# Optimization experiments

Hardware: AMD Instinct MI355X
Metric: run time of the kernel (lower is better)

Reference implementation:

```python
import jax, jax.numpy as jnp
import numpy as np


def setup_inputs() -> dict:
    key = jax.random.key(0)
    ks = jax.random.split(key, 12)
    B, N, Dv, E, H, V, T = 128, 196, 512, 512, 1024, 10000, 20
    s = 0.02  # small init scale for numerical stability
    f = lambda k, shp: (jax.random.normal(k, shp, jnp.float32) * s)
    return {
        "features": jax.random.normal(ks[0], (B, N, Dv), jnp.float32),
        "captions": jax.random.randint(ks[1], (B, T), 0, V),
        "W_init_h": f(ks[2], (H, Dv)),
        "W_init_c": f(ks[3], (H, Dv)),
        "W_attn_v": f(ks[4], (1, Dv)),
        "b_attn_v": jnp.zeros((1,), jnp.float32),
        "W_attn_h": f(ks[5], (1, H)),
        "b_attn_h": jnp.zeros((1,), jnp.float32),
        "embed_table": f(ks[6], (V, E)),
        "W_ih": f(ks[7], (4 * H, Dv + E)),
        "W_hh": f(ks[8], (4 * H, H)),
        "b_ih": jnp.zeros((4 * H,), jnp.float32),
        "b_hh": jnp.zeros((4 * H,), jnp.float32),
        "W_out": f(ks[9], (V, H)),
        "b_out": jnp.zeros((V,), jnp.float32),
    }


def reference(features, captions, W_init_h, W_init_c, W_attn_v, b_attn_v,
              W_attn_h, b_attn_h, embed_table, W_ih, W_hh, b_ih, b_hh,
              W_out, b_out):
    B, N, Dv = features.shape
    # _init_hidden: mean over vis_num of linear projections (division by vis_num)
    h0 = jnp.sum(jnp.einsum('bnd,hd->bnh', features, W_init_h), axis=1) / N
    c0 = jnp.sum(jnp.einsum('bnd,hd->bnh', features, W_init_c), axis=1) / N

    emb = embed_table[captions]                      # B,T,E
    emb_t_major = jnp.swapaxes(emb, 0, 1)            # T,B,E
    # visual attention logits are time-invariant; precompute once
    att_v = jnp.einsum('bnd,od->bno', features, W_attn_v) + b_attn_v  # B,N,1

    def step(carry, emb_t):
        h, c = carry
        # soft attention over vis_num locations
        att_h = (h @ W_attn_h.T + b_attn_h)[:, None, :]   # B,1,1
        alpha = jax.nn.softmax(att_v + att_h, axis=1)     # B,N,1
        ctx = jnp.sum(features * alpha, axis=1)           # B,Dv
        # single-step LSTM (PyTorch gate order: i, f, g, o)
        x = jnp.concatenate([ctx, emb_t], axis=-1)        # B,Dv+E
        gates = x @ W_ih.T + h @ W_hh.T + b_ih + b_hh     # B,4H
        i, fg, g, o = jnp.split(gates, 4, axis=-1)
        c_new = jax.nn.sigmoid(fg) * c + jax.nn.sigmoid(i) * jnp.tanh(g)
        h_new = jax.nn.sigmoid(o) * jnp.tanh(c_new)
        words = h_new @ W_out.T + b_out                   # B,V
        return (h_new, c_new), words

    _, word_space = jax.lax.scan(step, (h0, c0), emb_t_major)  # T,B,V
    # pack_padded_sequence with all-equal lengths flattens time-major -> (T*B, V)
    packed = word_space.reshape(-1, word_space.shape[-1])
    return jax.nn.log_softmax(packed, axis=1), jax.nn.softmax(packed, axis=1)
```

## Files before the change

### kernel.cpp

```cpp
#include <hip/hip_runtime.h>
#include <math.h>

#define B    128
#define NLOC 196
#define DV   512
#define EMB  512
#define HD   1024
#define VV   10000
#define TT   20
#define G4   4096
#define VPAD 10112
#define BH   (B*HD)

typedef short bf16x8 __attribute__((ext_vector_type(8)));
typedef float f32x4  __attribute__((ext_vector_type(4)));

__device__ __forceinline__ unsigned short f2bf(float x) {
    unsigned u = __builtin_bit_cast(unsigned, x);
    unsigned r = (u + 0x7fffu + ((u >> 16) & 1u)) >> 16;
    return (unsigned short)r;
}

__device__ __forceinline__ void gload_lds16(const void* g, void* lds) {
    __builtin_amdgcn_global_load_lds(
        (const __attribute__((address_space(1))) void*)g,
        (__attribute__((address_space(3))) void*)lds, 16, 0, 0);
}


__global__ void fmean_kernel(const float* __restrict__ feat, short* __restrict__ fmean_b) {
    int idx = blockIdx.x * blockDim.x + threadIdx.x;
    if (idx >= B * DV) return;
    int b = idx / DV, d = idx % DV;
    const float* p = feat + (size_t)b * NLOC * DV + d;
    float s = 0.f;
    for (int n = 0; n < NLOC; ++n) s += p[(size_t)n * DV];
    fmean_b[idx] = (short)f2bf(s * (1.0f / NLOC));
}

__global__ void attv_kernel(const float* __restrict__ feat, const float* __restrict__ wv,
                            const float* __restrict__ bv, float* __restrict__ attv) {
    int row  = blockIdx.x;
    int lane = threadIdx.x;
    const float* p = feat + (size_t)row * DV;
    float s = 0.f;
    for (int k = lane; k < DV; k += 64) s += p[k] * wv[k];
    for (int off = 32; off > 0; off >>= 1) s += __shfl_down(s, off);
    if (lane == 0) attv[row] = s + bv[0];
}

__global__ void alpha_kernel(const float* __restrict__ attv, float* __restrict__ alpha) {
    int b   = blockIdx.x;
    int tid = threadIdx.x;
    __shared__ float red[256];
    float v = (tid < NLOC) ? attv[b * NLOC + tid] : -1e30f;
    red[tid] = v; __syncthreads();
    for (int s = 128; s > 0; s >>= 1) { if (tid < s) red[tid] = fmaxf(red[tid], red[tid + s]); __syncthreads(); }
    float m = red[0]; __syncthreads();
    float e = (tid < NLOC) ? expf(v - m) : 0.f;
    red[tid] = e; __syncthreads();
    for (int s = 128; s > 0; s >>= 1) { if (tid < s) red[tid] += red[tid + s]; __syncthreads(); }
    float sum = red[0];
    if (tid < NLOC) alpha[b * NLOC + tid] = e / sum;
}

__global__ void ctx_kernel(const float* __restrict__ feat, const float* __restrict__ alpha,
                           short* __restrict__ ctx_b) {
    int idx = blockIdx.x * blockDim.x + threadIdx.x;
    if (idx >= B * DV) return;
    int b = idx / DV, d = idx % DV;
    const float* p = feat + (size_t)b * NLOC * DV + d;
    const float* a = alpha + b * NLOC;
    float s = 0.f;
    for (int n = 0; n < NLOC; ++n) s += a[n] * p[(size_t)n * DV];
    ctx_b[idx] = (short)f2bf(s);
}

__global__ void emb_gather_kernel(const int* __restrict__ captions, const float* __restrict__ table,
                                  short* __restrict__ emb_b) {
    size_t idx = (size_t)blockIdx.x * blockDim.x + threadIdx.x;
    if (idx >= (size_t)TT * B * EMB) return;
    int k = (int)(idx % EMB);
    int r = (int)(idx / EMB);
    int t = r / B, b = r % B;
    int cap = captions[b * TT + t];
    emb_b[idx] = (short)f2bf(table[(size_t)cap * EMB + k]);
}

__global__ void f2bf_pad_kernel(const float* __restrict__ in, short* __restrict__ out,
                                size_t n, size_t npad) {
    size_t i = (size_t)blockIdx.x * blockDim.x + threadIdx.x;
    if (i >= npad) return;
    out[i] = (i < n) ? (short)f2bf(in[i]) : (short)0;
}

__global__ void whh_perm_kernel(const float* __restrict__ in, short* __restrict__ out) {
    size_t idx = (size_t)blockIdx.x * blockDim.x + threadIdx.x;
    if (idx >= (size_t)G4 * HD) return;
    int k = (int)(idx & (HD - 1));
    int P = (int)(idx >> 10);
    int u = P >> 2, g = P & 3;
    out[idx] = (short)f2bf(in[(size_t)(g * HD + u) * HD + k]);
}

__global__ void hcvt_kernel(const float* __restrict__ h, short* __restrict__ h_bf) {
    int idx = blockIdx.x * blockDim.x + threadIdx.x;
    if (idx >= B * HD) return;
    h_bf[idx] = (short)f2bf(h[idx]);
}

template<int BN, int WR, int WC>
__global__ __launch_bounds__(256)
void gemm_bf16(const short* __restrict__ A, const short* __restrict__ Bw,
               float* __restrict__ C,
               const float* __restrict__ bias0, const float* __restrict__ bias1,
               int M, int N, int K, int lda, int ldb, int ldc) {
    constexpr int BM = 128;
    constexpr int BK = 32;
    constexpr int WM = BM / WR;
    constexpr int WN = BN / WC;
    constexpr int FM = WM / 16;
    constexpr int FN = WN / 16;
    __shared__ __align__(16) short As[BM * BK];
    __shared__ __align__(16) short Bs[BN * BK];
    const int tid  = threadIdx.x;
    const int wave = tid >> 6, lane = tid & 63;
    const int wr = wave / WC, wc = wave % WC;
    const int m0 = blockIdx.y * BM, n0 = blockIdx.x * BN;
    const int laneoff = lane * 16;

    f32x4 acc[FM][FN] = {};

    for (int k0 = 0; k0 < K; k0 += BK) {
        #pragma unroll
        for (int r = 0; r < 2; ++r) {
            int o   = r * 4096 + wave * 1024 + laneoff;
            int row = o >> 6;
            int col = (o & 63) >> 1;
            gload_lds16(A + (size_t)(m0 + row) * lda + k0 + col,
                        (char*)As + r * 4096 + wave * 1024);
        }
        constexpr int BBYTES = BN * BK * 2;
        if constexpr (BBYTES >= 4096) {
            #pragma unroll
            for (int r = 0; r < BBYTES / 4096; ++r) {
                int o   = r * 4096 + wave * 1024 + laneoff;
                int row = o >> 6;
                int col = (o & 63) >> 1;
                gload_lds16(Bw + (size_t)(n0 + row) * ldb + k0 + col,
                            (char*)Bs + r * 4096 + wave * 1024);
            }
        } else {
            constexpr int NW = BBYTES / 1024;
            if (wave < NW) {
                int o   = wave * 1024 + laneoff;
                int row = o >> 6;
                int col = (o & 63) >> 1;
                gload_lds16(Bw + (size_t)(n0 + row) * ldb + k0 + col,
                            (char*)Bs + wave * 1024);
            }
        }
        __syncthreads();

        bf16x8 a[FM], b[FN];
        const int kfr = (lane >> 4) * 8;
        #pragma unroll
        for (int i = 0; i < FM; ++i) {
            int row = wr * WM + i * 16 + (lane & 15);
            a[i] = *(const bf16x8*)&As[row * BK + kfr];
        }
        #pragma unroll
        for (int j = 0; j < FN; ++j) {
            int row = wc * WN + j * 16 + (lane & 15);
            b[j] = *(const bf16x8*)&Bs[row * BK + kfr];
        }
        #pragma unroll
        for (int i = 0; i < FM; ++i)
            #pragma unroll
            for (int j = 0; j < FN; ++j)
                acc[i][j] = __builtin_amdgcn_mfma_f32_16x16x32_bf16(a[i], b[j], acc[i][j], 0, 0, 0);
        __syncthreads();
    }

    #pragma unroll
    for (int i = 0; i < FM; ++i) {
        #pragma unroll
        for (int j = 0; j < FN; ++j) {
            int col = n0 + wc * WN + j * 16 + (lane & 15);
            if (col >= N) continue;
            float bv = (bias0 ? bias0[col] : 0.f) + (bias1 ? bias1[col] : 0.f);
            #pragma unroll
            for (int q = 0; q < 4; ++q) {
                int row = m0 + wr * WM + i * 16 + (lane >> 4) * 4 + q;
                if (row < M) C[(size_t)row * ldc + col] = acc[i][j][q] + bv;
            }
        }
    }
}

__global__ __launch_bounds__(256)
void lstm_step6(const short* __restrict__ Hprev, const short* __restrict__ Whh_p,
                const float* __restrict__ pre_t, const float* __restrict__ gctx,
                float* __restrict__ cbuf, short* __restrict__ Hnext,
                short* __restrict__ Hall_t) {
    __shared__ __align__(16) short As[64 * 512];
    __shared__ __align__(16) short Ws[32 * 512];
    __shared__ float gsm[4][64][8];
    const int tid  = threadIdx.x;
    const int lane = tid & 63, wave = tid >> 6;
    const int n0 = blockIdx.x * 32;
    const int m0 = blockIdx.y * 64;

    const int arowL = wave * 16 + (lane & 15);
    const int brow0 = lane & 15;
    const int brow1 = 16 + (lane & 15);
    const int kg    = lane >> 4;

    f32x4 acc0 = {}, acc1 = {};

    for (int h2 = 0; h2 < 2; ++h2) {
        const int k0 = h2 * 512;
        #pragma unroll
        for (int it = 0; it < 16; ++it) {
            int fg  = it * 256 + tid;
            int row = fg >> 6;
            int g   = fg & 63;
            int col = (g ^ (row & 7)) * 8;
            gload_lds16(Hprev + (size_t)(m0 + row) * HD + k0 + col,
                        (char*)As + it * 4096 + wave * 1024);
        }
        #pragma unroll
        for (int it = 0; it < 8; ++it) {
            int fg  = it * 256 + tid;
            int row = fg >> 6;
            int g   = fg & 63;
            int col = (g ^ (row & 7)) * 8;
            gload_lds16(Whh_p + (size_t)(n0 + row) * HD + k0 + col,
                        (char*)Ws + it * 4096 + wave * 1024);
        }
        __syncthreads();
        #pragma unroll
        for (int ks = 0; ks < 16; ++ks) {
            int lg = ks * 4 + kg;
            bf16x8 a  = *(const bf16x8*)((const char*)As + arowL * 1024 + ((lg ^ (arowL & 7)) << 4));
            bf16x8 w0 = *(const bf16x8*)((const char*)Ws + brow0 * 1024 + ((lg ^ (brow0 & 7)) << 4));
            bf16x8 w1 = *(const bf16x8*)((const char*)Ws + brow1 * 1024 + ((lg ^ (brow1 & 7)) << 4));
            acc0 = __builtin_amdgcn_mfma_f32_16x16x32_bf16(a, w0, acc0, 0, 0, 0);
            acc1 = __builtin_amdgcn_mfma_f32_16x16x32_bf16(a, w1, acc1, 0, 0, 0);
        }
        __syncthreads();
    }

    #pragma unroll
    for (int q = 0; q < 4; ++q) {
        int rr = wave * 16 + (lane >> 4) * 4 + q;
        int p0 = brow0, p1 = brow1;
        gsm[p0 & 3][rr][p0 >> 2] = acc0[q];
        gsm[p1 & 3][rr][p1 >> 2] = acc1[q];
    }
    __syncthreads();

    #pragma unroll
    for (int s = 0; s < 2; ++s) {
        int idx = tid + s * 256;
        int m = idx >> 3, u8 = idx & 7;
        int r = m0 + m, u = blockIdx.x * 8 + u8;
        size_t pb = (size_t)r * G4 + u;
        float gi  = gsm[0][m][u8] + pre_t[pb]          + gctx[pb];
        float gf  = gsm[1][m][u8] + pre_t[pb + HD]     + gctx[pb + HD];
        float gg2 = gsm[2][m][u8] + pre_t[pb + 2 * HD] + gctx[pb + 2 * HD];
        float go  = gsm[3][m][u8] + pre_t[pb + 3 * HD] + gctx[pb + 3 * HD];
        float si = 1.f / (1.f + expf(-gi));
        float sf = 1.f / (1.f + expf(-gf));
        float so = 1.f / (1.f + expf(-go));
        float cn = sf * cbuf[(size_t)r * HD + u] + si * tanhf(gg2);
        float hn = so * tanhf(cn);
        cbuf[(size_t)r * HD + u] = cn;
        short hb = (short)f2bf(hn);
        Hnext[(size_t)r * HD + u]  = hb;
        Hall_t[(size_t)r * HD + u] = hb;
    }
}

__global__ __launch_bounds__(512)
void softmax_kernel(float* __restrict__ words_logout, float* __restrict__ smout) {
    __shared__ float rowbuf[VV];
    __shared__ float red[512];
    int r = blockIdx.x;
    int tid = threadIdx.x;
    float* row = words_logout + (size_t)r * VV;
    float m = -1e30f;
    for (int i = tid; i < VV; i += 512) {
        float v = row[i];
        rowbuf[i] = v;
        m = fmaxf(m, v);
    }
    red[tid] = m; __syncthreads();
    for (int s = 256; s > 0; s >>= 1) { if (tid < s) red[tid] = fmaxf(red[tid], red[tid + s]); __syncthreads(); }
    m = red[0]; __syncthreads();
    float sum = 0.f;
    for (int i = tid; i < VV; i += 512) sum += expf(rowbuf[i] - m);
    red[tid] = sum; __syncthreads();
    for (int s = 256; s > 0; s >>= 1) { if (tid < s) red[tid] += red[tid + s]; __syncthreads(); }
    sum = red[0];
    float inv = 1.f / sum;
    float lz = logf(sum);
    for (int i = tid; i < VV; i += 512) {
        float x = rowbuf[i];
        smout[(size_t)r * VV + i] = expf(x - m) * inv;
        row[i] = x - m - lz;
    }
}

extern "C" void kernel_launch(void* const* d_in, const int* in_sizes, int n_in,
                              void* d_out, int out_size, void* d_ws, size_t ws_size,
                              hipStream_t stream) {
    const float* features    = (const float*)d_in[0];
    const int*   captions    = (const int*)  d_in[1];
    const float* W_init_h    = (const float*)d_in[2];
    const float* W_init_c    = (const float*)d_in[3];
    const float* W_attn_v    = (const float*)d_in[4];
    const float* b_attn_v    = (const float*)d_in[5];
    const float* embed_table = (const float*)d_in[8];
    const float* W_ih        = (const float*)d_in[9];
    const float* W_hh        = (const float*)d_in[10];
    const float* b_ih        = (const float*)d_in[11];
    const float* b_hh        = (const float*)d_in[12];
    const float* W_out       = (const float*)d_in[13];
    const float* b_out       = (const float*)d_in[14];

    float* out   = (float*)d_out;
    float* words = out;
    float* s2    = out + (size_t)TT * B * VV;

    float* gate_pre = s2;
    short* Hall_b   = (short*)(s2 + (size_t)10485760);
    short* Wout_b   = (short*)(s2 + (size_t)10485760 + 1310720);
    short* Wih_b    = Wout_b + (size_t)VPAD * HD;
    short* Whh_b    = Wih_b  + (size_t)G4 * HD;
    short* Wini_h_b = Whh_b  + (size_t)G4 * HD;
    short* Wini_c_b = Wini_h_b + (size_t)HD * DV;

    char* w = (char*)d_ws;
    size_t off = 0;
    auto alloc = [&](size_t bytes) { void* p = w + off; off = (off + bytes + 255) & ~255UL; return p; };
    float* attv   = (float*)alloc((size_t)B * NLOC * 4);
    float* alpha  = (float*)alloc((size_t)B * NLOC * 4);
    float* gctx   = (float*)alloc((size_t)B * G4 * 4);
    float* h0f    = (float*)alloc((size_t)B * HD * 4);
    float* cbuf   = (float*)alloc((size_t)B * HD * 4);
    short* fmean_b= (short*)alloc((size_t)B * DV * 2);
    short* ctx_b  = (short*)alloc((size_t)B * DV * 2);
    short* h_ping = (short*)alloc((size_t)B * HD * 2);
    short* h_pong = (short*)alloc((size_t)B * HD * 2);
    short* emb_b  = (short*)alloc((size_t)TT * B * EMB * 2);

    f2bf_pad_kernel<<<((size_t)VPAD * HD + 255) / 256, 256, 0, stream>>>(
        W_out, Wout_b, (size_t)VV * HD, (size_t)VPAD * HD);
    f2bf_pad_kernel<<<((size_t)G4 * HD + 255) / 256, 256, 0, stream>>>(
        W_ih, Wih_b, (size_t)G4 * HD, (size_t)G4 * HD);
    whh_perm_kernel<<<((size_t)G4 * HD + 255) / 256, 256, 0, stream>>>(W_hh, Whh_b);
    f2bf_pad_kernel<<<((size_t)HD * DV + 255) / 256, 256, 0, stream>>>(
        W_init_h, Wini_h_b, (size_t)HD * DV, (size_t)HD * DV);
    f2bf_pad_kernel<<<((size_t)HD * DV + 255) / 256, 256, 0, stream>>>(
        W_init_c, Wini_c_b, (size_t)HD * DV, (size_t)HD * DV);

    fmean_kernel<<<(B * DV + 255) / 256, 256, 0, stream>>>(features, fmean_b);
    attv_kernel<<<B * NLOC, 64, 0, stream>>>(features, W_attn_v, b_attn_v, attv);
    alpha_kernel<<<B, 256, 0, stream>>>(attv, alpha);
    ctx_kernel<<<(B * DV + 255) / 256, 256, 0, stream>>>(features, alpha, ctx_b);
    emb_gather_kernel<<<((size_t)TT * B * EMB + 255) / 256, 256, 0, stream>>>(captions, embed_table, emb_b);

    gemm_bf16<32, 4, 1><<<dim3(HD / 32, 1), 256, 0, stream>>>(
        fmean_b, Wini_h_b, h0f, nullptr, nullptr, B, HD, DV, DV, DV, HD);
    gemm_bf16<32, 4, 1><<<dim3(HD / 32, 1), 256, 0, stream>>>(
        fmean_b, Wini_c_b, cbuf, nullptr, nullptr, B, HD, DV, DV, DV, HD);
    hcvt_kernel<<<(B * HD + 255) / 256, 256, 0, stream>>>(h0f, h_ping);

    gemm_bf16<32, 4, 1><<<dim3(G4 / 32, 1), 256, 0, stream>>>(
        ctx_b, Wih_b, gctx, b_ih, b_hh, B, G4, DV, DV, HD, G4);
    gemm_bf16<128, 2, 2><<<dim3(G4 / 128, TT * B / 128), 256, 0, stream>>>(
        emb_b, Wih_b + DV, gate_pre, nullptr, nullptr, TT * B, G4, EMB, EMB, DV + EMB, G4);

    for (int t = 0; t < TT; ++t) {
        lstm_step6<<<dim3(G4 / 32, B / 64), 256, 0, stream>>>(
            (t & 1) ? h_pong : h_ping, Whh_b, gate_pre + (size_t)t * B * G4, gctx,
            cbuf, (t & 1) ? h_ping : h_pong, Hall_b + (size_t)t * BH);
    }

    gemm_bf16<128, 2, 2><<<dim3(VPAD / 128, TT * B / 128), 256, 0, stream>>>(
        Hall_b, Wout_b, words, b_out, nullptr, TT * B, VV, HD, HD, HD, VV);
    softmax_kernel<<<TT * B, 512, 0, stream>>>(words, s2);
}
```

Measured before the change: 493.0 us.

## Fuse LSTM time loop into persistent cooperative kernel with LDS-resident weights

Replaces the 20 per-timestep LSTM kernel launches with a single cooperative kernel of 256 blocks that loops over time and uses grid.sync() between steps. Each block loads its 32-row W_hh slice into LDS once and keeps it there for all steps. The cell state stays in registers instead of round-tripping through global memory. This removes per-step launch overhead and repeated weight loads. In exchange it relies on grid-wide barrier latency and on all 256 blocks being co-resident, with a larger LDS footprint per block.

```diff
diff --git a/kernel.cpp b/kernel.cpp
--- a/kernel.cpp
+++ b/kernel.cpp
@@ -1,5 +1,8 @@
 #include <hip/hip_runtime.h>
+#include <hip/hip_cooperative_groups.h>
 #include <math.h>
+
+namespace cg = cooperative_groups;
 
 #define B    128
 #define NLOC 196
@@ -199,86 +202,117 @@
 }
 
 __global__ __launch_bounds__(256)
-void lstm_step6(const short* __restrict__ Hprev, const short* __restrict__ Whh_p,
-                const float* __restrict__ pre_t, const float* __restrict__ gctx,
-                float* __restrict__ cbuf, short* __restrict__ Hnext,
-                short* __restrict__ Hall_t) {
+void lstm_persist(const short* __restrict__ H0, const short* __restrict__ Whh_p,
+                  const float* __restrict__ gate_pre, const float* __restrict__ gctx,
+                  const float* __restrict__ cbuf,
+                  short* __restrict__ h_ping, short* __restrict__ h_pong,
+                  short* __restrict__ Hall_b) {
+    __shared__ __align__(16) short Ws[32 * 1024];
     __shared__ __align__(16) short As[64 * 512];
-    __shared__ __align__(16) short Ws[32 * 512];
     __shared__ float gsm[4][64][8];
+    cg::grid_group grid = cg::this_grid();
+
     const int tid  = threadIdx.x;
     const int lane = tid & 63, wave = tid >> 6;
-    const int n0 = blockIdx.x * 32;
-    const int m0 = blockIdx.y * 64;
+    const int bid  = blockIdx.x;
+    const int nx = bid & 127, my = bid >> 7;
+    const int n0 = nx * 32;
+    const int m0 = my * 64;
+
+    #pragma unroll
+    for (int it = 0; it < 16; ++it) {
+        int fg  = it * 256 + tid;
+        int row = fg >> 7;
+        int g   = fg & 127;
+        int col = (g ^ (row & 7)) * 8;
+        gload_lds16(Whh_p + (size_t)(n0 + row) * HD + col,
+                    (char*)Ws + it * 4096 + wave * 1024);
+    }
 
     const int arowL = wave * 16 + (lane & 15);
     const int brow0 = lane & 15;
     const int brow1 = 16 + (lane & 15);
     const int kg    = lane >> 4;
 
-    f32x4 acc0 = {}, acc1 = {};
-
-    for (int h2 = 0; h2 < 2; ++h2) {
-        const int k0 = h2 * 512;
-        #pragma unroll
-        for (int it = 0; it < 16; ++it) {
-            int fg  = it * 256 + tid;
-            int row = fg >> 6;
-            int g   = fg & 63;
-            int col = (g ^ (row & 7)) * 8;
-            gload_lds16(Hprev + (size_t)(m0 + row) * HD + k0 + col,
-                        (char*)As + it * 4096 + wave * 1024);
-        }
-        #pragma unroll
-        for (int it = 0; it < 8; ++it) {
-            int fg  = it * 256 + tid;
-            int row = fg >> 6;
-            int g   = fg & 63;
-            int col = (g ^ (row & 7)) * 8;
-            gload_lds16(Whh_p + (size_t)(n0 + row) * HD + k0 + col,
-                        (char*)Ws + it * 4096 + wave * 1024);
+    const int m_a = tid >> 3,           u8_a = tid & 7;
+    const int m_b = (tid + 256) >> 3,   u8_b = (tid + 256) & 7;
+    const int r_a = m0 + m_a, u_a = nx * 8 + u8_a;
+    const int r_b = m0 + m_b, u_b = nx * 8 + u8_b;
+    float c_a = cbuf[(size_t)r_a * HD + u_a];
+    float c_b = cbuf[(size_t)r_b * HD + u_b];
+
+    for (int t = 0; t < TT; ++t) {
+        const short* Hprev = (t == 0) ? H0 : ((t & 1) ? h_pong : h_ping);
+        short* Hnext = (t & 1) ? h_ping : h_pong;
+        const float* pre_t = gate_pre + (size_t)t * B * G4;
+        f32x4 acc0 = {}, acc1 = {};
+
+        #pragma unroll
+        for (int h2 = 0; h2 < 2; ++h2) {
+            const int k0 = h2 * 512;
+            #pragma unroll
+            for (int it = 0; it < 16; ++it) {
+                int fg  = it * 256 + tid;
+                int row = fg >> 6;
+                int g   = fg & 63;
+                int col = (g ^ (row & 7)) * 8;
+                gload_lds16(Hprev + (size_t)(m0 + row) * HD + k0 + col,
+                            (char*)As + it * 4096 + wave * 1024);
+            }
+            __syncthreads();
+            #pragma unroll
+            for (int ks = 0; ks < 16; ++ks) {
+                int lgA = ks * 4 + kg;
+                int lgW = h2 * 64 + ks * 4 + kg;
+                bf16x8 a  = *(const bf16x8*)((const char*)As + arowL * 1024 + ((lgA ^ (arowL & 7)) << 4));
+                bf16x8 w0 = *(const bf16x8*)((const char*)Ws + brow0 * 2048 + ((lgW ^ (brow0 & 7)) << 4));
+                bf16x8 w1 = *(const bf16x8*)((const char*)Ws + brow1 * 2048 + ((lgW ^ (brow1 & 7)) << 4));
+                acc0 = __builtin_amdgcn_mfma_f32_16x16x32_bf16(a, w0, acc0, 0, 0, 0);
+                acc1 = __builtin_amdgcn_mfma_f32_16x16x32_bf16(a, w1, acc1, 0, 0, 0);
+            }
+            __syncthreads();
+        }
+
+        #pragma unroll
+        for (int q = 0; q < 4; ++q) {
+            int rr = wave * 16 + (lane >> 4) * 4 + q;
+            gsm[brow0 & 3][rr][brow0 >> 2] = acc0[q];
+            gsm[brow1 & 3][rr][brow1 >> 2] = acc1[q];
         }
         __syncthreads();
-        #pragma unroll
-        for (int ks = 0; ks < 16; ++ks) {
-            int lg = ks * 4 + kg;
-            bf16x8 a  = *(const bf16x8*)((const char*)As + arowL * 1024 + ((lg ^ (arowL & 7)) << 4));
-            bf16x8 w0 = *(const bf16x8*)((const char*)Ws + brow0 * 1024 + ((lg ^ (brow0 & 7)) << 4));
-            bf16x8 w1 = *(const bf16x8*)((const char*)Ws + brow1 * 1024 + ((lg ^ (brow1 & 7)) << 4));
-            acc0 = __builtin_amdgcn_mfma_f32_16x16x32_bf16(a, w0, acc0, 0, 0, 0);
-            acc1 = __builtin_amdgcn_mfma_f32_16x16x32_bf16(a, w1, acc1, 0, 0, 0);
-        }
-        __syncthreads();
-    }
-
-    #pragma unroll
-    for (int q = 0; q < 4; ++q) {
-        int rr = wave * 16 + (lane >> 4) * 4 + q;
-        int p0 = brow0, p1 = brow1;
-        gsm[p0 & 3][rr][p0 >> 2] = acc0[q];
-        gsm[p1 & 3][rr][p1 >> 2] = acc1[q];
-    }
-    __syncthreads();
-
-    #pragma unroll
-    for (int s = 0; s < 2; ++s) {
-        int idx = tid + s * 256;
-        int m = idx >> 3, u8 = idx & 7;
-        int r = m0 + m, u = blockIdx.x * 8 + u8;
-        size_t pb = (size_t)r * G4 + u;
-        float gi  = gsm[0][m][u8] + pre_t[pb]          + gctx[pb];
-        float gf  = gsm[1][m][u8] + pre_t[pb + HD]     + gctx[pb + HD];
-        float gg2 = gsm[2][m][u8] + pre_t[pb + 2 * HD] + gctx[pb + 2 * HD];
-        float go  = gsm[3][m][u8] + pre_t[pb + 3 * HD] + gctx[pb + 3 * HD];
-        float si = 1.f / (1.f + expf(-gi));
-        float sf = 1.f / (1.f + expf(-gf));
-        float so = 1.f / (1.f + expf(-go));
-        float cn = sf * cbuf[(size_t)r * HD + u] + si * tanhf(gg2);
-        float hn = so * tanhf(cn);
-        cbuf[(size_t)r * HD + u] = cn;
-        short hb = (short)f2bf(hn);
-        Hnext[(size_t)r * HD + u]  = hb;
-        Hall_t[(size_t)r * HD + u] = hb;
+
+        {
+            size_t pb = (size_t)r_a * G4 + u_a;
+            float gi  = gsm[0][m_a][u8_a] + pre_t[pb]          + gctx[pb];
+            float gf  = gsm[1][m_a][u8_a] + pre_t[pb + HD]     + gctx[pb + HD];
+            float gg2 = gsm[2][m_a][u8_a] + pre_t[pb + 2 * HD] + gctx[pb + 2 * HD];
+            float go  = gsm[3][m_a][u8_a] + pre_t[pb + 3 * HD] + gctx[pb + 3 * HD];
+            float si = 1.f / (1.f + expf(-gi));
+            float sf = 1.f / (1.f + expf(-gf));
+            float so = 1.f / (1.f + expf(-go));
+            c_a = sf * c_a + si * tanhf(gg2);
+            float hn = so * tanhf(c_a);
+            short hb = (short)f2bf(hn);
+            Hnext[(size_t)r_a * HD + u_a] = hb;
+            Hall_b[(size_t)t * BH + (size_t)r_a * HD + u_a] = hb;
+        }
+        {
+            size_t pb = (size_t)r_b * G4 + u_b;
+            float gi  = gsm[0][m_b][u8_b] + pre_t[pb]          + gctx[pb];
+            float gf  = gsm[1][m_b][u8_b] + pre_t[pb + HD]     + gctx[pb + HD];
+            float gg2 = gsm[2][m_b][u8_b] + pre_t[pb + 2 * HD] + gctx[pb + 2 * HD];
+            float go  = gsm[3][m_b][u8_b] + pre_t[pb + 3 * HD] + gctx[pb + 3 * HD];
+            float si = 1.f / (1.f + expf(-gi));
+            float sf = 1.f / (1.f + expf(-gf));
+            float so = 1.f / (1.f + expf(-go));
+            c_b = sf * c_b + si * tanhf(gg2);
+            float hn = so * tanhf(c_b);
+            short hb = (short)f2bf(hn);
+            Hnext[(size_t)r_b * HD + u_b] = hb;
+            Hall_b[(size_t)t * BH + (size_t)r_b * HD + u_b] = hb;
+        }
+
+        grid.sync();
     }
 }
 
@@ -382,10 +416,12 @@
     gemm_bf16<128, 2, 2><<<dim3(G4 / 128, TT * B / 128), 256, 0, stream>>>(
         emb_b, Wih_b + DV, gate_pre, nullptr, nullptr, TT * B, G4, EMB, EMB, DV + EMB, G4);
 
-    for (int t = 0; t < TT; ++t) {
-        lstm_step6<<<dim3(G4 / 32, B / 64), 256, 0, stream>>>(
-            (t & 1) ? h_pong : h_ping, Whh_b, gate_pre + (size_t)t * B * G4, gctx,
-            cbuf, (t & 1) ? h_ping : h_pong, Hall_b + (size_t)t * BH);
+    {
+        const short* H0 = h_ping;
+        void* args[] = { (void*)&H0, (void*)&Whh_b, (void*)&gate_pre, (void*)&gctx,
+                         (void*)&cbuf, (void*)&h_ping, (void*)&h_pong, (void*)&Hall_b };
+        hipLaunchCooperativeKernel((void*)lstm_persist, dim3(256), dim3(256),
+                                   args, 0, stream);
     }
 
     gemm_bf16<128, 2, 2><<<dim3(VPAD / 128, TT * B / 128), 256, 0, stream>>>(
```

After: 1.066 ms. 116% more time.

## Double-buffer K chunks in LSTM recurrent step to overlap loads with MFMA

Applied to the files above, without the earlier changes.

The per-timestep LSTM kernel now splits the K=1024 reduction into four 256-wide chunks instead of two 512-wide ones. It ping-pongs two LDS buffers so the global-to-LDS loads for the next chunk are issued before the MFMAs on the current chunk. The goal is to hide global-load latency in the recurrent H·W_hh product, which the serial time loop repeats 20 times. Total LDS use stays the same, but there are more barriers per block, and the end-of-iteration barrier may wait on the in-flight loads and so limit the overlap.

```diff
diff --git a/kernel.cpp b/kernel.cpp
--- a/kernel.cpp
+++ b/kernel.cpp
@@ -199,12 +199,12 @@
 }
 
 __global__ __launch_bounds__(256)
-void lstm_step6(const short* __restrict__ Hprev, const short* __restrict__ Whh_p,
+void lstm_step7(const short* __restrict__ Hprev, const short* __restrict__ Whh_p,
                 const float* __restrict__ pre_t, const float* __restrict__ gctx,
                 float* __restrict__ cbuf, short* __restrict__ Hnext,
                 short* __restrict__ Hall_t) {
-    __shared__ __align__(16) short As[64 * 512];
-    __shared__ __align__(16) short Ws[32 * 512];
+    __shared__ __align__(16) short As[2][64 * 256];
+    __shared__ __align__(16) short Ws[2][32 * 256];
     __shared__ float gsm[4][64][8];
     const int tid  = threadIdx.x;
     const int lane = tid & 63, wave = tid >> 6;
@@ -216,35 +216,46 @@
     const int brow1 = 16 + (lane & 15);
     const int kg    = lane >> 4;
 
-    f32x4 acc0 = {}, acc1 = {};
-
-    for (int h2 = 0; h2 < 2; ++h2) {
-        const int k0 = h2 * 512;
-        #pragma unroll
-        for (int it = 0; it < 16; ++it) {
+    auto stageA = [&](int q, int buf) {
+        const int k0 = q * 256;
+        #pragma unroll
+        for (int it = 0; it < 8; ++it) {
             int fg  = it * 256 + tid;
-            int row = fg >> 6;
-            int g   = fg & 63;
+            int row = fg >> 5;
+            int g   = fg & 31;
             int col = (g ^ (row & 7)) * 8;
             gload_lds16(Hprev + (size_t)(m0 + row) * HD + k0 + col,
-                        (char*)As + it * 4096 + wave * 1024);
-        }
-        #pragma unroll
-        for (int it = 0; it < 8; ++it) {
+                        (char*)As[buf] + it * 4096 + wave * 1024);
+        }
+    };
+    auto stageW = [&](int q, int buf) {
+        const int k0 = q * 256;
+        #pragma unroll
+        for (int it = 0; it < 4; ++it) {
             int fg  = it * 256 + tid;
-            int row = fg >> 6;
-            int g   = fg & 63;
+            int row = fg >> 5;
+            int g   = fg & 31;
             int col = (g ^ (row & 7)) * 8;
             gload_lds16(Whh_p + (size_t)(n0 + row) * HD + k0 + col,
-                        (char*)Ws + it * 4096 + wave * 1024);
-        }
-        __syncthreads();
-        #pragma unroll
-        for (int ks = 0; ks < 16; ++ks) {
+                        (char*)Ws[buf] + it * 4096 + wave * 1024);
+        }
+    };
+
+    f32x4 acc0 = {}, acc1 = {};
+
+    stageA(0, 0); stageW(0, 0);
+    __syncthreads();
+
+    #pragma unroll
+    for (int q = 0; q < 4; ++q) {
+        const int cur = q & 1;
+        if (q + 1 < 4) { stageA(q + 1, cur ^ 1); stageW(q + 1, cur ^ 1); }
+        #pragma unroll
+        for (int ks = 0; ks < 8; ++ks) {
             int lg = ks * 4 + kg;
-            bf16x8 a  = *(const bf16x8*)((const char*)As + arowL * 1024 + ((lg ^ (arowL & 7)) << 4));
-            bf16x8 w0 = *(const bf16x8*)((const char*)Ws + brow0 * 1024 + ((lg ^ (brow0 & 7)) << 4));
-            bf16x8 w1 = *(const bf16x8*)((const char*)Ws + brow1 * 1024 + ((lg ^ (brow1 & 7)) << 4));
+            bf16x8 a  = *(const bf16x8*)((const char*)As[cur] + arowL * 512 + ((lg ^ (arowL & 7)) << 4));
+            bf16x8 w0 = *(const bf16x8*)((const char*)Ws[cur] + brow0 * 512 + ((lg ^ (brow0 & 7)) << 4));
+            bf16x8 w1 = *(const bf16x8*)((const char*)Ws[cur] + brow1 * 512 + ((lg ^ (brow1 & 7)) << 4));
             acc0 = __builtin_amdgcn_mfma_f32_16x16x32_bf16(a, w0, acc0, 0, 0, 0);
             acc1 = __builtin_amdgcn_mfma_f32_16x16x32_bf16(a, w1, acc1, 0, 0, 0);
         }
@@ -254,9 +265,8 @@
     #pragma unroll
     for (int q = 0; q < 4; ++q) {
         int rr = wave * 16 + (lane >> 4) * 4 + q;
-        int p0 = brow0, p1 = brow1;
-        gsm[p0 & 3][rr][p0 >> 2] = acc0[q];
-        gsm[p1 & 3][rr][p1 >> 2] = acc1[q];
+        gsm[brow0 & 3][rr][brow0 >> 2] = acc0[q];
+        gsm[brow1 & 3][rr][brow1 >> 2] = acc1[q];
     }
     __syncthreads();
 
@@ -383,7 +393,7 @@
         emb_b, Wih_b + DV, gate_pre, nullptr, nullptr, TT * B, G4, EMB, EMB, DV + EMB, G4);
 
     for (int t = 0; t < TT; ++t) {
-        lstm_step6<<<dim3(G4 / 32, B / 64), 256, 0, stream>>>(
+        lstm_step7<<<dim3(G4 / 32, B / 64), 256, 0, stream>>>(
             (t & 1) ? h_pong : h_ping, Whh_b, gate_pre + (size_t)t * B * G4, gctx,
             cbuf, (t & 1) ? h_ping : h_pong, Hall_b + (size_t)t * BH);
     }
```

Result: slower. 519.9 us (+5.5%).
